# Performance work log

Measured on AMD Instinct MI355X. Metric: run time of the kernel, lower is better.

## Reference

```python
import jax, jax.numpy as jnp
import numpy as np

D_MODEL = 1024
NHEAD = 16
HEAD_DIM = D_MODEL // NHEAD
B, T = 4, 2048


def setup_inputs() -> dict:
    key = jax.random.key(0)
    ks = jax.random.split(key, 5)
    s = 0.02
    return {
        "x": jax.random.normal(ks[0], (B, T, D_MODEL), dtype=jnp.float32),
        "w_qkv": jax.random.normal(ks[1], (D_MODEL, 3 * D_MODEL), dtype=jnp.float32) * s,
        "b_qkv": jnp.zeros((3 * D_MODEL,), dtype=jnp.float32),
        "w_proj": jax.random.normal(ks[2], (D_MODEL, D_MODEL), dtype=jnp.float32) * s,
        "b_proj": jnp.zeros((D_MODEL,), dtype=jnp.float32),
    }


def reference(x, w_qkv, b_qkv, w_proj, b_proj):
    Bx, Tx, D = x.shape
    qkv = x @ w_qkv + b_qkv                      # [B,T,3D]
    qkv = qkv.reshape(Bx, Tx, 3, NHEAD, HEAD_DIM)
    q, k, v = qkv[:, :, 0], qkv[:, :, 1], qkv[:, :, 2]   # [B,T,H,hd]
    q = q.transpose(0, 2, 1, 3)                  # [B,H,T,hd]
    k = k.transpose(0, 2, 1, 3)
    v = v.transpose(0, 2, 1, 3)
    scale = 1.0 / jnp.sqrt(jnp.asarray(HEAD_DIM, dtype=x.dtype))
    attn = jnp.einsum("bhqd,bhkd->bhqk", q, k) * scale   # [B,H,T,T]
    causal = jnp.tril(jnp.ones((Tx, Tx), dtype=bool))
    attn = jnp.where(causal[None, None], attn, jnp.asarray(-jnp.inf, dtype=attn.dtype))
    attn = jax.nn.softmax(attn, axis=-1)
    # dropout p=0.0 (eval / identity)
    out = jnp.einsum("bhqk,bhkd->bhqd", attn, v)          # [B,H,T,hd]
    out = out.transpose(0, 2, 1, 3).reshape(Bx, Tx, D)
    return out @ w_proj + b_proj
```

## Files before the change

kernel.cpp:

```cpp
#include <hip/hip_runtime.h>
#include <hip/hip_bf16.h>
#include <math.h>

#define D_MODEL 1024
#define NH      16
#define HD      64
#define T_SEQ   2048
#define B_SZ    4
#define M_ROWS  (B_SZ * T_SEQ)
#define N_QKV   (3 * D_MODEL)

typedef __bf16 bf16x8 __attribute__((ext_vector_type(8)));
typedef __bf16 bf16x4 __attribute__((ext_vector_type(4)));
typedef float  f32x4  __attribute__((ext_vector_type(4)));

__device__ __forceinline__ bf16x8 cvt8(float4 a, float4 b) {
    bf16x8 v;
    v[0]=(__bf16)a.x; v[1]=(__bf16)a.y; v[2]=(__bf16)a.z; v[3]=(__bf16)a.w;
    v[4]=(__bf16)b.x; v[5]=(__bf16)b.y; v[6]=(__bf16)b.z; v[7]=(__bf16)b.w;
    return v;
}

__device__ __forceinline__ void gload_lds16(const __bf16* g, __bf16* l) {
    __builtin_amdgcn_global_load_lds(
        (const __attribute__((address_space(1))) void*)g,
        (__attribute__((address_space(3))) void*)l, 16, 0, 0);
}

__device__ __forceinline__ float exp2v(float x) {
    float r;
    asm("v_exp_f32 %0, %1" : "=v"(r) : "v"(x));
    return r;
}

__global__ __launch_bounds__(256) void cvt_bf16(const float* __restrict__ in,
                                                __bf16* __restrict__ out, int n8)
{
    int i = blockIdx.x * 256 + threadIdx.x;
    if (i < n8) {
        float4 a = ((const float4*)in)[2 * i];
        float4 b = ((const float4*)in)[2 * i + 1];
        ((bf16x8*)out)[i] = cvt8(a, b);
    }
}

__global__ __launch_bounds__(256) void transpose_cvt(
    const float* __restrict__ W, __bf16* __restrict__ WT, int R, int C)
{
    __shared__ float t[32][33];
    const int tr0 = blockIdx.y * 32, tc0 = blockIdx.x * 32;
    const int lr = threadIdx.x >> 5, lc = threadIdx.x & 31;
    #pragma unroll
    for (int i = 0; i < 4; ++i)
        t[lr + i * 8][lc] = W[(size_t)(tr0 + lr + i * 8) * C + tc0 + lc];
    __syncthreads();
    #pragma unroll
    for (int i = 0; i < 4; ++i)
        WT[(size_t)(tc0 + lr + i * 8) * R + tr0 + lc] = (__bf16)t[lc][lr + i * 8];
}

template<int MODE>
__global__ __launch_bounds__(256) void gemm_mfma(
    const __bf16* __restrict__ A, const __bf16* __restrict__ BT,
    const float* __restrict__ bias, void* __restrict__ C0,
    __bf16* __restrict__ vT, int M, int N, int K)
{
    __shared__ __bf16 As[128 * 64];
    __shared__ __bf16 Bs[128 * 64];

    const int nbn = N >> 7;
    const int nwg = gridDim.x;
    int bid = blockIdx.x;
    bid = (bid & 7) * (nwg >> 3) + (bid >> 3);
    const int tm = bid / nbn, tn = bid % nbn;
    const int row0 = tm << 7, col0 = tn << 7;

    const int tid  = threadIdx.x;
    const int wid  = tid >> 6, lane = tid & 63;
    const int wm   = wid >> 1, wn = wid & 1;
    const int g    = lane >> 4, r16 = lane & 15;

    f32x4 acc[4][4] = {};

    for (int k0 = 0; k0 < K; k0 += 64) {
        #pragma unroll
        for (int i = 0; i < 4; ++i) {
            const int seg = wid * 4 + i;
            const int row = seg * 8 + (lane >> 3);
            const int kel = ((lane & 7) * 8) ^ ((row & 7) * 8);
            gload_lds16(A  + (size_t)(row0 + row) * K + k0 + kel, As + seg * 512);
            gload_lds16(BT + (size_t)(col0 + row) * K + k0 + kel, Bs + seg * 512);
        }
        __syncthreads();

        #pragma unroll
        for (int kk = 0; kk < 2; ++kk) {
            bf16x8 af[4], bfr[4];
            #pragma unroll
            for (int mt = 0; mt < 4; ++mt) {
                const int row = wm * 64 + mt * 16 + r16;
                af[mt] = *(const bf16x8*)((const char*)As + row * 128
                             + ((kk * 64 + g * 16) ^ ((row & 7) << 4)));
            }
            #pragma unroll
            for (int nt = 0; nt < 4; ++nt) {
                const int row = wn * 64 + nt * 16 + r16;
                bfr[nt] = *(const bf16x8*)((const char*)Bs + row * 128
                             + ((kk * 64 + g * 16) ^ ((row & 7) << 4)));
            }
            #pragma unroll
            for (int mt = 0; mt < 4; ++mt)
                #pragma unroll
                for (int nt = 0; nt < 4; ++nt)
                    acc[mt][nt] = __builtin_amdgcn_mfma_f32_16x16x32_bf16(
                        af[mt], bfr[nt], acc[mt][nt], 0, 0, 0);
        }
        __syncthreads();
    }

    const bool isV = (MODE == 1) && (tn >= 16);

    #pragma unroll
    for (int mt = 0; mt < 4; ++mt) {
        #pragma unroll
        for (int nt = 0; nt < 4; ++nt) {
            const int col = col0 + wn * 64 + nt * 16 + r16;
            const float bv = bias[col];
            const int rowb = row0 + wm * 64 + mt * 16 + g * 4;
            if (MODE == 0) {
                #pragma unroll
                for (int j = 0; j < 4; ++j)
                    ((float*)C0)[(size_t)(rowb + j) * N + col] = acc[mt][nt][j] + bv;
            } else if (!isV) {
                #pragma unroll
                for (int j = 0; j < 4; ++j)
                    ((__bf16*)C0)[(size_t)(rowb + j) * 2048 + col] =
                        (__bf16)(acc[mt][nt][j] + bv);
            } else {
                const int hh = (col - 2048) >> 6, dd = (col - 2048) & 63;
                const int bb = rowb >> 11, tt = rowb & 2047;
                __bf16 p4[4];
                #pragma unroll
                for (int j = 0; j < 4; ++j) p4[j] = (__bf16)(acc[mt][nt][j] + bv);
                *(bf16x4*)&vT[((size_t)((bb * NH + hh) * HD + dd)) * T_SEQ + tt]
                    = *(const bf16x4*)p4;
            }
        }
    }
}

__global__ __launch_bounds__(128) void attn_mfma(
    const __bf16* __restrict__ qkb, const __bf16* __restrict__ vT,
    __bf16* __restrict__ aout)
{
    const int idx  = blockIdx.x;
    const int s    = idx >> 6;
    const int qt   = (s & 4) ? ((s >> 3) * 4 + (s & 3))
                             : (31 - (s >> 3) * 4 - (s & 3));
    const int bh   = idx & 63;
    const int b    = bh >> 4;
    const int h    = bh & 15;
    const int tid  = threadIdx.x;
    const int wid  = tid >> 6;
    const int lane = tid & 63;
    const int g    = lane >> 4;
    const int n    = lane & 15;
    const int swzn = (n & 7) << 4;

    const int q0    = qt * 64;
    const int qbase = q0 + wid * 32;
    const int nkt   = qt + 1;

    __shared__ __align__(16) char Ks[64 * 128];
    __shared__ __align__(16) char Vs[64 * 128];
    __shared__ __align__(16) char Ps[2][32 * 128];

    const int srow = tid >> 1;
    const int sch2 = tid & 1;
    const int swzw = (srow & 7) << 4;

    const float qscale = 0.125f * 1.44269504089f;
    bf16x8 qa[2][2];
    #pragma unroll
    for (int rb = 0; rb < 2; ++rb) {
        const size_t qrow = (size_t)(b * T_SEQ + qbase + rb * 16 + n) * 2048
                            + (size_t)h * HD;
        qa[rb][0] = *(const bf16x8*)&qkb[qrow + g * 8];
        qa[rb][1] = *(const bf16x8*)&qkb[qrow + 32 + g * 8];
        #pragma unroll
        for (int jj = 0; jj < 8; ++jj) {
            qa[rb][0][jj] = (__bf16)((float)qa[rb][0][jj] * qscale);
            qa[rb][1][jj] = (__bf16)((float)qa[rb][1][jj] * qscale);
        }
    }

    f32x4 o[2][4] = {};
    float mrow[2][4] = {};
    float lrow[2][4] = {};

    const __bf16* gK = qkb + (size_t)(b * T_SEQ + srow) * 2048 + 1024
                       + (size_t)h * HD + sch2 * 32;
    const __bf16* gV = vT + ((size_t)((b * NH + h) * HD + srow)) * T_SEQ + sch2 * 32;

    bf16x8 kreg[4], vreg[4];
    #pragma unroll
    for (int c = 0; c < 4; ++c) {
        kreg[c] = *(const bf16x8*)(gK + c * 8);
        vreg[c] = *(const bf16x8*)(gV + c * 8);
    }

    for (int kt = 0; kt < nkt; ++kt) {
        #pragma unroll
        for (int c = 0; c < 4; ++c) {
            const int boff = (sch2 * 64 + c * 16) ^ swzw;
            *(bf16x8*)(Ks + srow * 128 + boff) = kreg[c];
            *(bf16x8*)(Vs + srow * 128 + boff) = vreg[c];
        }
        __syncthreads();

        if (kt + 1 < nkt) {
            const size_t kb2 = (size_t)(kt + 1) * 64;
            #pragma unroll
            for (int c = 0; c < 4; ++c) {
                kreg[c] = *(const bf16x8*)(gK + kb2 * 2048 + c * 8);
                vreg[c] = *(const bf16x8*)(gV + kb2 + c * 8);
            }
        }

        const int kb0 = kt * 64;

        f32x4 s4[2][4] = {};
        __builtin_amdgcn_s_setprio(1);
        #pragma unroll
        for (int cc = 0; cc < 2; ++cc) {
            bf16x8 kf[4];
            #pragma unroll
            for (int sub = 0; sub < 4; ++sub)
                kf[sub] = *(const bf16x8*)(Ks + (sub * 16 + n) * 128
                                           + ((cc * 64 + g * 16) ^ swzn));
            #pragma unroll
            for (int rb = 0; rb < 2; ++rb)
                #pragma unroll
                for (int sub = 0; sub < 4; ++sub)
                    s4[rb][sub] = __builtin_amdgcn_mfma_f32_16x16x32_bf16(
                        qa[rb][cc], kf[sub], s4[rb][sub], 0, 0, 0);
        }
        __builtin_amdgcn_s_setprio(0);

        const bool needmask = (kb0 + 63 > qbase);

        #pragma unroll
        for (int rb = 0; rb < 2; ++rb) {
            if (needmask) {
                #pragma unroll
                for (int r = 0; r < 4; ++r) {
                    const int qrow = qbase + rb * 16 + 4 * g + r;
                    #pragma unroll
                    for (int sub = 0; sub < 4; ++sub)
                        if (kb0 + sub * 16 + n > qrow) s4[rb][sub][r] = -INFINITY;
                }
            }
            float pm[4];
            int ok = 1;
            #pragma unroll
            for (int r = 0; r < 4; ++r) {
                pm[r] = fmaxf(fmaxf(s4[rb][0][r], s4[rb][1][r]),
                              fmaxf(s4[rb][2][r], s4[rb][3][r]));
                ok &= (pm[r] <= mrow[rb][r] + 8.f);
            }
            if (__all(ok)) {
                #pragma unroll
                for (int r = 0; r < 4; ++r) {
                    const float m = mrow[rb][r];
                    const float p0 = exp2v(s4[rb][0][r] - m);
                    const float p1 = exp2v(s4[rb][1][r] - m);
                    const float p2 = exp2v(s4[rb][2][r] - m);
                    const float p3 = exp2v(s4[rb][3][r] - m);
                    lrow[rb][r] += (p0 + p1) + (p2 + p3);
                    char* prow = Ps[wid] + (rb * 16 + 4 * g + r) * 128;
                    const int pswz = ((4 * g + r) & 7) << 4;
                    *(__bf16*)(prow + ((2 * n)      ^ pswz)) = (__bf16)p0;
                    *(__bf16*)(prow + ((2 * n + 32) ^ pswz)) = (__bf16)p1;
                    *(__bf16*)(prow + ((2 * n + 64) ^ pswz)) = (__bf16)p2;
                    *(__bf16*)(prow + ((2 * n + 96) ^ pswz)) = (__bf16)p3;
                }
            } else {
                #pragma unroll
                for (int r = 0; r < 4; ++r) {
                    float tm = pm[r];
                    #pragma unroll
                    for (int off = 1; off < 16; off <<= 1)
                        tm = fmaxf(tm, __shfl_xor(tm, off));
                    const float mnew = fmaxf(mrow[rb][r], tm);
                    const float corr = exp2v(mrow[rb][r] - mnew);
                    mrow[rb][r] = mnew;
                    const float p0 = exp2v(s4[rb][0][r] - mnew);
                    const float p1 = exp2v(s4[rb][1][r] - mnew);
                    const float p2 = exp2v(s4[rb][2][r] - mnew);
                    const float p3 = exp2v(s4[rb][3][r] - mnew);
                    lrow[rb][r] = lrow[rb][r] * corr + (p0 + p1) + (p2 + p3);
                    #pragma unroll
                    for (int nt = 0; nt < 4; ++nt) o[rb][nt][r] *= corr;
                    char* prow = Ps[wid] + (rb * 16 + 4 * g + r) * 128;
                    const int pswz = ((4 * g + r) & 7) << 4;
                    *(__bf16*)(prow + ((2 * n)      ^ pswz)) = (__bf16)p0;
                    *(__bf16*)(prow + ((2 * n + 32) ^ pswz)) = (__bf16)p1;
                    *(__bf16*)(prow + ((2 * n + 64) ^ pswz)) = (__bf16)p2;
                    *(__bf16*)(prow + ((2 * n + 96) ^ pswz)) = (__bf16)p3;
                }
            }
        }

        __builtin_amdgcn_s_setprio(1);
        #pragma unroll
        for (int cc = 0; cc < 2; ++cc) {
            bf16x8 vf[4];
            #pragma unroll
            for (int nt = 0; nt < 4; ++nt)
                vf[nt] = *(const bf16x8*)(Vs + (nt * 16 + n) * 128
                                          + ((cc * 64 + g * 16) ^ swzn));
            #pragma unroll
            for (int rb = 0; rb < 2; ++rb) {
                bf16x8 pa = *(const bf16x8*)(Ps[wid] + (rb * 16 + n) * 128
                                             + ((cc * 64 + g * 16) ^ swzn));
                #pragma unroll
                for (int nt = 0; nt < 4; ++nt)
                    o[rb][nt] = __builtin_amdgcn_mfma_f32_16x16x32_bf16(
                        pa, vf[nt], o[rb][nt], 0, 0, 0);
            }
        }
        __builtin_amdgcn_s_setprio(0);
        __syncthreads();
    }

    #pragma unroll
    for (int rb = 0; rb < 2; ++rb) {
        float inv[4];
        #pragma unroll
        for (int r = 0; r < 4; ++r) {
            float ssum = lrow[rb][r];
            #pragma unroll
            for (int off = 1; off < 16; off <<= 1)
                ssum += __shfl_xor(ssum, off);
            inv[r] = 1.f / ssum;
        }
        const size_t obase = (size_t)(b * T_SEQ + qbase + rb * 16) * D_MODEL
                             + (size_t)h * HD;
        #pragma unroll
        for (int nt = 0; nt < 4; ++nt)
            #pragma unroll
            for (int r = 0; r < 4; ++r)
                aout[obase + (size_t)(4 * g + r) * D_MODEL + nt * 16 + n]
                    = (__bf16)(o[rb][nt][r] * inv[r]);
    }
}

extern "C" void kernel_launch(void* const* d_in, const int* in_sizes, int n_in,
                              void* d_out, int out_size, void* d_ws, size_t ws_size,
                              hipStream_t stream)
{
    const float* x      = (const float*)d_in[0];
    const float* w_qkv  = (const float*)d_in[1];
    const float* b_qkv  = (const float*)d_in[2];
    const float* w_proj = (const float*)d_in[3];
    const float* b_proj = (const float*)d_in[4];
    float* out = (float*)d_out;

    char* ws = (char*)d_ws;
    __bf16* qkb    = (__bf16*)ws;
    __bf16* vTb    = qkb + (size_t)M_ROWS * 2048;
    __bf16* xb     = vTb + (size_t)NH * B_SZ * HD * T_SEQ;
    __bf16* wqkvT  = xb + (size_t)M_ROWS * D_MODEL;
    __bf16* wprojT = wqkvT + (size_t)N_QKV * D_MODEL;
    __bf16* aout   = wprojT + (size_t)D_MODEL * D_MODEL;

    cvt_bf16<<<dim3(M_ROWS * D_MODEL / 8 / 256), 256, 0, stream>>>(
        x, xb, M_ROWS * D_MODEL / 8);
    transpose_cvt<<<dim3(N_QKV / 32, D_MODEL / 32), 256, 0, stream>>>(
        w_qkv, wqkvT, D_MODEL, N_QKV);
    transpose_cvt<<<dim3(D_MODEL / 32, D_MODEL / 32), 256, 0, stream>>>(
        w_proj, wprojT, D_MODEL, D_MODEL);

    gemm_mfma<1><<<dim3((M_ROWS / 128) * (N_QKV / 128)), 256, 0, stream>>>(
        xb, wqkvT, b_qkv, qkb, vTb, M_ROWS, N_QKV, D_MODEL);

    attn_mfma<<<dim3(B_SZ * NH * 32), 128, 0, stream>>>(qkb, vTb, aout);

    gemm_mfma<0><<<dim3((M_ROWS / 128) * (D_MODEL / 128)), 256, 0, stream>>>(
        aout, wprojT, b_proj, out, nullptr, M_ROWS, D_MODEL, D_MODEL);
}
```

Baseline: 203.7 us.

## Double attention query tile to 128 rows per block with 64 rows per warp

Each attention block now handles 128 query rows instead of 64, with each of two warps owning 64 rows (four 16-row MFMA tiles), so every K/V tile staged in shared memory is reused across twice as many queries. The launch grid is halved and the causal tile schedule is remapped to pair heavy and light query tiles. In the last K tile, warp 0 skips compute through an active flag. This raises register and LDS pressure and halves the number of blocks, which may lower occupancy and worsen load balance across CUs.

```diff
diff --git a/kernel.cpp b/kernel.cpp
--- a/kernel.cpp
+++ b/kernel.cpp
@@ -154,9 +154,9 @@
     __bf16* __restrict__ aout)
 {
     const int idx  = blockIdx.x;
-    const int s    = idx >> 6;
-    const int qt   = (s & 4) ? ((s >> 3) * 4 + (s & 3))
-                             : (31 - (s >> 3) * 4 - (s & 3));
+    const int slot = idx >> 6;
+    const int j    = slot & 3, p = slot >> 2;
+    const int qt   = (p == 0) ? 15 - j : (p == 1) ? 8 + j : (p == 2) ? 4 + j : 3 - j;
     const int bh   = idx & 63;
     const int b    = bh >> 4;
     const int h    = bh & 15;
@@ -167,22 +167,22 @@
     const int n    = lane & 15;
     const int swzn = (n & 7) << 4;
 
-    const int q0    = qt * 64;
-    const int qbase = q0 + wid * 32;
-    const int nkt   = qt + 1;
+    const int q0    = qt * 128;
+    const int qbase = q0 + wid * 64;
+    const int nkt   = 2 * qt + 2;
 
     __shared__ __align__(16) char Ks[64 * 128];
     __shared__ __align__(16) char Vs[64 * 128];
-    __shared__ __align__(16) char Ps[2][32 * 128];
+    __shared__ __align__(16) char Ps[2][64 * 128];
 
     const int srow = tid >> 1;
     const int sch2 = tid & 1;
     const int swzw = (srow & 7) << 4;
 
     const float qscale = 0.125f * 1.44269504089f;
-    bf16x8 qa[2][2];
-    #pragma unroll
-    for (int rb = 0; rb < 2; ++rb) {
+    bf16x8 qa[4][2];
+    #pragma unroll
+    for (int rb = 0; rb < 4; ++rb) {
         const size_t qrow = (size_t)(b * T_SEQ + qbase + rb * 16 + n) * 2048
                             + (size_t)h * HD;
         qa[rb][0] = *(const bf16x8*)&qkb[qrow + g * 8];
@@ -194,9 +194,9 @@
         }
     }
 
-    f32x4 o[2][4] = {};
-    float mrow[2][4] = {};
-    float lrow[2][4] = {};
+    f32x4 o[4][4] = {};
+    float mrow[4][4] = {};
+    float lrow[4][4] = {};
 
     const __bf16* gK = qkb + (size_t)(b * T_SEQ + srow) * 2048 + 1024
                        + (size_t)h * HD + sch2 * 32;
@@ -228,113 +228,116 @@
         }
 
         const int kb0 = kt * 64;
-
-        f32x4 s4[2][4] = {};
-        __builtin_amdgcn_s_setprio(1);
-        #pragma unroll
-        for (int cc = 0; cc < 2; ++cc) {
-            bf16x8 kf[4];
-            #pragma unroll
-            for (int sub = 0; sub < 4; ++sub)
-                kf[sub] = *(const bf16x8*)(Ks + (sub * 16 + n) * 128
-                                           + ((cc * 64 + g * 16) ^ swzn));
-            #pragma unroll
-            for (int rb = 0; rb < 2; ++rb)
+        const bool active = (kb0 <= qbase + 63);
+
+        if (active) {
+            bf16x8 kf[2][4];
+            #pragma unroll
+            for (int cc = 0; cc < 2; ++cc)
                 #pragma unroll
                 for (int sub = 0; sub < 4; ++sub)
-                    s4[rb][sub] = __builtin_amdgcn_mfma_f32_16x16x32_bf16(
-                        qa[rb][cc], kf[sub], s4[rb][sub], 0, 0, 0);
-        }
-        __builtin_amdgcn_s_setprio(0);
-
-        const bool needmask = (kb0 + 63 > qbase);
-
-        #pragma unroll
-        for (int rb = 0; rb < 2; ++rb) {
-            if (needmask) {
+                    kf[cc][sub] = *(const bf16x8*)(Ks + (sub * 16 + n) * 128
+                                                   + ((cc * 64 + g * 16) ^ swzn));
+
+            const bool needmask = (kb0 + 63 > qbase);
+
+            #pragma unroll
+            for (int rb = 0; rb < 4; ++rb) {
+                f32x4 s4[4] = {};
+                __builtin_amdgcn_s_setprio(1);
+                #pragma unroll
+                for (int cc = 0; cc < 2; ++cc)
+                    #pragma unroll
+                    for (int sub = 0; sub < 4; ++sub)
+                        s4[sub] = __builtin_amdgcn_mfma_f32_16x16x32_bf16(
+                            qa[rb][cc], kf[cc][sub], s4[sub], 0, 0, 0);
+                __builtin_amdgcn_s_setprio(0);
+
+                if (needmask) {
+                    #pragma unroll
+                    for (int r = 0; r < 4; ++r) {
+                        const int qrow = qbase + rb * 16 + 4 * g + r;
+                        #pragma unroll
+                        for (int sub = 0; sub < 4; ++sub)
+                            if (kb0 + sub * 16 + n > qrow) s4[sub][r] = -INFINITY;
+                    }
+                }
+                float pm[4];
+                int ok = 1;
                 #pragma unroll
                 for (int r = 0; r < 4; ++r) {
-                    const int qrow = qbase + rb * 16 + 4 * g + r;
-                    #pragma unroll
-                    for (int sub = 0; sub < 4; ++sub)
-                        if (kb0 + sub * 16 + n > qrow) s4[rb][sub][r] = -INFINITY;
+                    pm[r] = fmaxf(fmaxf(s4[0][r], s4[1][r]),
+                                  fmaxf(s4[2][r], s4[3][r]));
+                    ok &= (pm[r] <= mrow[rb][r] + 8.f);
                 }
-            }
-            float pm[4];
-            int ok = 1;
-            #pragma unroll
-            for (int r = 0; r < 4; ++r) {
-                pm[r] = fmaxf(fmaxf(s4[rb][0][r], s4[rb][1][r]),
-                              fmaxf(s4[rb][2][r], s4[rb][3][r]));
-                ok &= (pm[r] <= mrow[rb][r] + 8.f);
-            }
-            if (__all(ok)) {
-                #pragma unroll
-                for (int r = 0; r < 4; ++r) {
-                    const float m = mrow[rb][r];
-                    const float p0 = exp2v(s4[rb][0][r] - m);
-                    const float p1 = exp2v(s4[rb][1][r] - m);
-                    const float p2 = exp2v(s4[rb][2][r] - m);
-                    const float p3 = exp2v(s4[rb][3][r] - m);
-                    lrow[rb][r] += (p0 + p1) + (p2 + p3);
-                    char* prow = Ps[wid] + (rb * 16 + 4 * g + r) * 128;
-                    const int pswz = ((4 * g + r) & 7) << 4;
-                    *(__bf16*)(prow + ((2 * n)      ^ pswz)) = (__bf16)p0;
-                    *(__bf16*)(prow + ((2 * n + 32) ^ pswz)) = (__bf16)p1;
-                    *(__bf16*)(prow + ((2 * n + 64) ^ pswz)) = (__bf16)p2;
-                    *(__bf16*)(prow + ((2 * n + 96) ^ pswz)) = (__bf16)p3;
+                if (__all(ok)) {
+                    #pragma unroll
+                    for (int r = 0; r < 4; ++r) {
+                        const float m = mrow[rb][r];
+                        const float p0 = exp2v(s4[0][r] - m);
+                        const float p1 = exp2v(s4[1][r] - m);
+                        const float p2 = exp2v(s4[2][r] - m);
+                        const float p3 = exp2v(s4[3][r] - m);
+                        lrow[rb][r] += (p0 + p1) + (p2 + p3);
+                        char* prow = Ps[wid] + (rb * 16 + 4 * g + r) * 128;
+                        const int pswz = ((4 * g + r) & 7) << 4;
+                        *(__bf16*)(prow + ((2 * n)      ^ pswz)) = (__bf16)p0;
+                        *(__bf16*)(prow + ((2 * n + 32) ^ pswz)) = (__bf16)p1;
+                        *(__bf16*)(prow + ((2 * n + 64) ^ pswz)) = (__bf16)p2;
+                        *(__bf16*)(prow + ((2 * n + 96) ^ pswz)) = (__bf16)p3;
+                    }
+                } else {
+                    #pragma unroll
+                    for (int r = 0; r < 4; ++r) {
+                        float tm = pm[r];
+                        #pragma unroll
+                        for (int off = 1; off < 16; off <<= 1)
+                            tm = fmaxf(tm, __shfl_xor(tm, off));
+                        const float mnew = fmaxf(mrow[rb][r], tm);
+                        const float corr = exp2v(mrow[rb][r] - mnew);
+                        mrow[rb][r] = mnew;
+                        const float p0 = exp2v(s4[0][r] - mnew);
+                        const float p1 = exp2v(s4[1][r] - mnew);
+                        const float p2 = exp2v(s4[2][r] - mnew);
+                        const float p3 = exp2v(s4[3][r] - mnew);
+                        lrow[rb][r] = lrow[rb][r] * corr + (p0 + p1) + (p2 + p3);
+                        #pragma unroll
+                        for (int nt = 0; nt < 4; ++nt) o[rb][nt][r] *= corr;
+                        char* prow = Ps[wid] + (rb * 16 + 4 * g + r) * 128;
+                        const int pswz = ((4 * g + r) & 7) << 4;
+                        *(__bf16*)(prow + ((2 * n)      ^ pswz)) = (__bf16)p0;
+                        *(__bf16*)(prow + ((2 * n + 32) ^ pswz)) = (__bf16)p1;
+                        *(__bf16*)(prow + ((2 * n + 64) ^ pswz)) = (__bf16)p2;
+                        *(__bf16*)(prow + ((2 * n + 96) ^ pswz)) = (__bf16)p3;
+                    }
                 }
-            } else {
-                #pragma unroll
-                for (int r = 0; r < 4; ++r) {
-                    float tm = pm[r];
-                    #pragma unroll
-                    for (int off = 1; off < 16; off <<= 1)
-                        tm = fmaxf(tm, __shfl_xor(tm, off));
-                    const float mnew = fmaxf(mrow[rb][r], tm);
-                    const float corr = exp2v(mrow[rb][r] - mnew);
-                    mrow[rb][r] = mnew;
-                    const float p0 = exp2v(s4[rb][0][r] - mnew);
-                    const float p1 = exp2v(s4[rb][1][r] - mnew);
-                    const float p2 = exp2v(s4[rb][2][r] - mnew);
-                    const float p3 = exp2v(s4[rb][3][r] - mnew);
-                    lrow[rb][r] = lrow[rb][r] * corr + (p0 + p1) + (p2 + p3);
-                    #pragma unroll
-                    for (int nt = 0; nt < 4; ++nt) o[rb][nt][r] *= corr;
-                    char* prow = Ps[wid] + (rb * 16 + 4 * g + r) * 128;
-                    const int pswz = ((4 * g + r) & 7) << 4;
-                    *(__bf16*)(prow + ((2 * n)      ^ pswz)) = (__bf16)p0;
-                    *(__bf16*)(prow + ((2 * n + 32) ^ pswz)) = (__bf16)p1;
-                    *(__bf16*)(prow + ((2 * n + 64) ^ pswz)) = (__bf16)p2;
-                    *(__bf16*)(prow + ((2 * n + 96) ^ pswz)) = (__bf16)p3;
+            }
+
+            __builtin_amdgcn_s_setprio(1);
+            #pragma unroll
+            for (int cc = 0; cc < 2; ++cc) {
+                bf16x8 vf[4];
+                #pragma unroll
+                for (int nt = 0; nt < 4; ++nt)
+                    vf[nt] = *(const bf16x8*)(Vs + (nt * 16 + n) * 128
+                                              + ((cc * 64 + g * 16) ^ swzn));
+                #pragma unroll
+                for (int rb = 0; rb < 4; ++rb) {
+                    bf16x8 pa = *(const bf16x8*)(Ps[wid] + (rb * 16 + n) * 128
+                                                 + ((cc * 64 + g * 16) ^ swzn));
+                    #pragma unroll
+                    for (int nt = 0; nt < 4; ++nt)
+                        o[rb][nt] = __builtin_amdgcn_mfma_f32_16x16x32_bf16(
+                            pa, vf[nt], o[rb][nt], 0, 0, 0);
                 }
             }
-        }
-
-        __builtin_amdgcn_s_setprio(1);
-        #pragma unroll
-        for (int cc = 0; cc < 2; ++cc) {
-            bf16x8 vf[4];
-            #pragma unroll
-            for (int nt = 0; nt < 4; ++nt)
-                vf[nt] = *(const bf16x8*)(Vs + (nt * 16 + n) * 128
-                                          + ((cc * 64 + g * 16) ^ swzn));
-            #pragma unroll
-            for (int rb = 0; rb < 2; ++rb) {
-                bf16x8 pa = *(const bf16x8*)(Ps[wid] + (rb * 16 + n) * 128
-                                             + ((cc * 64 + g * 16) ^ swzn));
-                #pragma unroll
-                for (int nt = 0; nt < 4; ++nt)
-                    o[rb][nt] = __builtin_amdgcn_mfma_f32_16x16x32_bf16(
-                        pa, vf[nt], o[rb][nt], 0, 0, 0);
-            }
-        }
-        __builtin_amdgcn_s_setprio(0);
+            __builtin_amdgcn_s_setprio(0);
+        }
         __syncthreads();
     }
 
     #pragma unroll
-    for (int rb = 0; rb < 2; ++rb) {
+    for (int rb = 0; rb < 4; ++rb) {
         float inv[4];
         #pragma unroll
         for (int r = 0; r < 4; ++r) {
@@ -384,7 +387,7 @@
     gemm_mfma<1><<<dim3((M_ROWS / 128) * (N_QKV / 128)), 256, 0, stream>>>(
         xb, wqkvT, b_qkv, qkb, vTb, M_ROWS, N_QKV, D_MODEL);
 
-    attn_mfma<<<dim3(B_SZ * NH * 32), 128, 0, stream>>>(qkb, vTb, aout);
+    attn_mfma<<<dim3(B_SZ * NH * 16), 128, 0, stream>>>(qkb, vTb, aout);
 
     gemm_mfma<0><<<dim3((M_ROWS / 128) * (D_MODEL / 128)), 256, 0, stream>>>(
         aout, wprojT, b_proj, out, nullptr, M_ROWS, D_MODEL, D_MODEL);
```

Measured after the change: 224.9 us. +10.4%, slower.
